# Kernel optimization log

Measured on AMD Instinct MI355X. Metric: run time of the kernel, lower is better.

Reference implementation:

```python
import jax, jax.numpy as jnp
import numpy as np

N_NODES, N_EDGES = 20000, 2000
IN_FEATS, NUM_HEADS, OUT_FEATS, EDGE_DIM = 128, 4, 32, 64
NEG_SLOPE = 0.2


def setup_inputs() -> dict:
    key = jax.random.key(0)
    ks = jax.random.split(key, 5)
    # Unique (node, edge) incidence pairs, concrete at setup time.
    rng = np.random.default_rng(0)
    flat = np.unique(rng.integers(0, N_NODES * N_EDGES, size=220000))
    src_idx = jnp.asarray(flat // N_EDGES, dtype=jnp.int32)
    edge_idx = jnp.asarray(flat % N_EDGES, dtype=jnp.int32)
    H = jnp.zeros((N_NODES, N_EDGES), jnp.float32).at[src_idx, edge_idx].set(1.0)
    feat = jax.random.normal(ks[0], (N_NODES, IN_FEATS), jnp.float32)
    edge_feat = jax.random.normal(ks[1], (N_EDGES, EDGE_DIM), jnp.float32)
    fc_w = jax.random.normal(ks[2], (IN_FEATS, NUM_HEADS * OUT_FEATS), jnp.float32) * 0.1
    attn_src = jax.random.normal(ks[3], (1, NUM_HEADS, OUT_FEATS), jnp.float32) * 0.1
    attn_edge = jax.random.normal(ks[4], (1, NUM_HEADS, EDGE_DIM), jnp.float32) * 0.1
    return {"feat": feat, "edge_feat": edge_feat, "H": H, "fc_w": fc_w,
            "attn_src": attn_src, "attn_edge": attn_edge,
            "src_idx": src_idx, "edge_idx": edge_idx}


def reference(feat, edge_feat, H, fc_w, attn_src, attn_edge, src_idx, edge_idx):
    n_nodes = feat.shape[0]
    n_edges = H.shape[1]
    # node projection -> [N, h, d]
    feat_src = (feat @ fc_w).reshape(n_nodes, NUM_HEADS, OUT_FEATS)
    # gather per incidence pair
    src_feat = feat_src[src_idx]                       # [P, h, d]
    e_src = (src_feat * attn_src).sum(-1)              # [P, h]
    e_edge = (edge_feat[edge_idx][:, None, :] * attn_edge).sum(-1)  # [P, h]
    e = jax.nn.leaky_relu(e_src + e_edge, NEG_SLOPE)   # [P, h]
    # grouped (per-hyperedge) softmax via segment ops
    max_val = jax.ops.segment_max(e, edge_idx, num_segments=n_edges)  # [E, h]
    e_exp = jnp.exp(e - max_val[edge_idx])
    sum_exp = jax.ops.segment_sum(e_exp, edge_idx, num_segments=n_edges)
    attention = e_exp / (sum_exp[edge_idx] + 1e-9)     # [P, h]
    # aggregate messages onto hyperedges
    messages = src_feat * attention[..., None]         # [P, h, d]
    hyper_edge_feats = jax.ops.segment_sum(messages, edge_idx, num_segments=n_edges)  # [E, h, d]
    # dense disseminate back to nodes
    rst = jnp.einsum('ne,ehd->nhd', H, hyper_edge_feats)
    return rst.reshape(n_nodes, NUM_HEADS * OUT_FEATS)
```

## Files before the change

### kernel.cpp

```cpp
#include <hip/hip_runtime.h>
#include <hip/hip_bf16.h>

#define N_NODES 20000
#define N_EDGES 2000
#define IN_FEATS 128
#define NUM_HEADS 4
#define OUT_FEATS 32
#define EDGE_DIM 64
#define C_FEATS 128
#define NEG_SLOPE 0.2f
#define MAXD 256
#define WT_LD 136
#define NTILES (N_NODES / 16)
#define PROJ_BLKS ((NTILES + 3) / 4)
#define K1_BLK 512
#define K1_THR 256
#define CUR_STRIDE 16

typedef __attribute__((ext_vector_type(8))) short bf16x8;
typedef __attribute__((ext_vector_type(4))) float f32x4;

__device__ __forceinline__ float leaky(float x) { return (x > 0.f) ? x : NEG_SLOPE * x; }
__device__ __forceinline__ short f2bf(float x) {
    __hip_bfloat16 h = __float2bfloat16(x);
    return *reinterpret_cast<short*>(&h);
}

__global__ __launch_bounds__(K1_THR) void proj_scatter_kernel(
    const float* __restrict__ feat, const float* __restrict__ fc_w,
    const float* __restrict__ attn_src,
    const int* __restrict__ src_idx, const int* __restrict__ edge_idx, int P,
    __hip_bfloat16* __restrict__ feat_bf, float* __restrict__ s_buf,
    int* __restrict__ cursor, int* __restrict__ node_start, int* __restrict__ edge_nodes)
{
    __shared__ unsigned short Wt[128 * WT_LD];
    const int t = threadIdx.x;
    const int bid = blockIdx.x;

    if (bid < PROJ_BLKS) {
        for (int q = t; q < 64 * 128; q += K1_THR) {
            const int c = q & 127, k = (q >> 7) * 2;
            Wt[c * WT_LD + k]     = (unsigned short)f2bf(fc_w[k * C_FEATS + c]);
            Wt[c * WT_LD + k + 1] = (unsigned short)f2bf(fc_w[(k + 1) * C_FEATS + c]);
        }
        __syncthreads();

        const int wave = t >> 6, lane = t & 63;
        const int wid = bid * 4 + wave;
        if (wid < NTILES) {
            const int m0 = wid * 16;
            const int lrow = lane & 15, lk = lane >> 4;

            bf16x8 afr[4];
            const float* arow = feat + (size_t)(m0 + lrow) * IN_FEATS + lk * 8;
            #pragma unroll
            for (int kt = 0; kt < 4; ++kt) {
                const float4 f0 = *(const float4*)(arow + kt * 32);
                const float4 f1 = *(const float4*)(arow + kt * 32 + 4);
                bf16x8 a;
                a[0] = f2bf(f0.x); a[1] = f2bf(f0.y); a[2] = f2bf(f0.z); a[3] = f2bf(f0.w);
                a[4] = f2bf(f1.x); a[5] = f2bf(f1.y); a[6] = f2bf(f1.z); a[7] = f2bf(f1.w);
                afr[kt] = a;
            }

            f32x4 acc[8];
            #pragma unroll
            for (int nt = 0; nt < 8; ++nt) acc[nt] = (f32x4){0.f, 0.f, 0.f, 0.f};
            #pragma unroll
            for (int nt = 0; nt < 8; ++nt) {
                const unsigned short* wrow = &Wt[(nt * 16 + lrow) * WT_LD + lk * 8];
                #pragma unroll
                for (int kt = 0; kt < 4; ++kt) {
                    const bf16x8 b = *(const bf16x8*)(wrow + kt * 32);
                    acc[nt] = __builtin_amdgcn_mfma_f32_16x16x32_bf16(afr[kt], b, acc[nt], 0, 0, 0);
                }
            }

            #pragma unroll
            for (int nt = 0; nt < 8; ++nt) {
                const int c = nt * 16 + lrow;
                #pragma unroll
                for (int r = 0; r < 4; ++r)
                    feat_bf[(size_t)(m0 + lk * 4 + r) * C_FEATS + c] = __float2bfloat16(acc[nt][r]);
            }
            float aw[8];
            #pragma unroll
            for (int nt = 0; nt < 8; ++nt) aw[nt] = attn_src[nt * 16 + lrow];
            #pragma unroll
            for (int h = 0; h < NUM_HEADS; ++h) {
                #pragma unroll
                for (int r = 0; r < 4; ++r) {
                    float v = acc[2 * h][r] * aw[2 * h] + acc[2 * h + 1][r] * aw[2 * h + 1];
                    v += __shfl_xor(v, 1);
                    v += __shfl_xor(v, 2);
                    v += __shfl_xor(v, 4);
                    v += __shfl_xor(v, 8);
                    if (lrow == 0) s_buf[(m0 + lk * 4 + r) * NUM_HEADS + h] = v;
                }
            }
        }
    } else {
        const int nthreads = (K1_BLK - PROJ_BLKS) * K1_THR;
        for (int p = (bid - PROJ_BLKS) * K1_THR + t; p < P; p += nthreads) {
            const int e = edge_idx[p];
            const int s = src_idx[p];
            const int pos = atomicAdd(&cursor[e * CUR_STRIDE], 1);
            if (pos < MAXD) edge_nodes[e * MAXD + pos] = s;
            const int prev = (p == 0) ? -1 : src_idx[p - 1];
            for (int n = prev + 1; n <= s; ++n) node_start[n] = p;
            if (p == P - 1)
                for (int n = s + 1; n <= N_NODES; ++n) node_start[n] = P;
        }
    }
}

__global__ __launch_bounds__(256) void edge_attn_kernel(
    const float* __restrict__ s_buf, const float* __restrict__ edge_feat,
    const float* __restrict__ attn_edge, const __hip_bfloat16* __restrict__ feat_bf,
    const int* __restrict__ cursor, const int* __restrict__ edge_nodes,
    float* __restrict__ hef)
{
    __shared__ float4 w_sh[MAXD];
    __shared__ int    n_sh[MAXD];
    __shared__ float  te_sh[NUM_HEADS];
    __shared__ float  inv_sh[NUM_HEADS];
    __shared__ float  wred[4][NUM_HEADS];
    __shared__ float  red[4][C_FEATS];

    const int e = blockIdx.x;
    const int t = threadIdx.x;
    const int wv = t >> 6, lane = t & 63;

    if (t < EDGE_DIM) {
        const float v = edge_feat[e * EDGE_DIM + t];
        #pragma unroll
        for (int h = 0; h < NUM_HEADS; ++h) {
            float p = v * attn_edge[h * EDGE_DIM + t];
            p += __shfl_xor(p, 32); p += __shfl_xor(p, 16); p += __shfl_xor(p, 8);
            p += __shfl_xor(p, 4);  p += __shfl_xor(p, 2);  p += __shfl_xor(p, 1);
            if (t == 0) te_sh[h] = p;
        }
    }
    __syncthreads();

    const int m = min(cursor[e * CUR_STRIDE], MAXD);
    const int m_pad = (m + 31) & ~31;

    float ps0 = 0.f, ps1 = 0.f, ps2 = 0.f, ps3 = 0.f;
    if (t < m) {
        const int n = edge_nodes[e * MAXD + t];
        n_sh[t] = n;
        const float4 s4 = *(const float4*)&s_buf[n * NUM_HEADS];
        float4 w;
        w.x = __expf(leaky(s4.x + te_sh[0]));
        w.y = __expf(leaky(s4.y + te_sh[1]));
        w.z = __expf(leaky(s4.z + te_sh[2]));
        w.w = __expf(leaky(s4.w + te_sh[3]));
        w_sh[t] = w;
        ps0 = w.x; ps1 = w.y; ps2 = w.z; ps3 = w.w;
    } else if (t < m_pad) {
        n_sh[t] = 0;
        w_sh[t] = make_float4(0.f, 0.f, 0.f, 0.f);
    }
    #pragma unroll
    for (int d = 32; d >= 1; d >>= 1) {
        ps0 += __shfl_xor(ps0, d); ps1 += __shfl_xor(ps1, d);
        ps2 += __shfl_xor(ps2, d); ps3 += __shfl_xor(ps3, d);
    }
    if (lane == 0) {
        wred[wv][0] = ps0; wred[wv][1] = ps1; wred[wv][2] = ps2; wred[wv][3] = ps3;
    }
    __syncthreads();
    if (t < NUM_HEADS)
        inv_sh[t] = 1.f / (wred[0][t] + wred[1][t] + wred[2][t] + wred[3][t] + 1e-9f);
    __syncthreads();

    const int c0 = lane * 2;
    const int h = lane >> 4;
    float a0 = 0.f, a1 = 0.f;
    const unsigned short* fb = (const unsigned short*)feat_bf;
    #pragma unroll 8
    for (int j = wv; j < m_pad; j += 4) {
        const int n = n_sh[j];
        const float w = ((const float*)&w_sh[j])[h];
        const unsigned v = *(const unsigned*)(fb + (size_t)n * C_FEATS + c0);
        a0 += w * __uint_as_float(v << 16);
        a1 += w * __uint_as_float(v & 0xffff0000u);
    }
    red[wv][c0] = a0;
    red[wv][c0 + 1] = a1;
    __syncthreads();
    if (t < C_FEATS) {
        const float r = red[0][t] + red[1][t] + red[2][t] + red[3][t];
        hef[e * C_FEATS + t] = r * inv_sh[t >> 5];
    }
}

#define K3_NODES 8
#define K3_CHUNK 512
__global__ __launch_bounds__(128) void disseminate_kernel(
    const int* __restrict__ node_start, const int* __restrict__ edge_idx,
    const float* __restrict__ hef, float* __restrict__ out)
{
    __shared__ int e_sh[K3_CHUNK];
    __shared__ int ns_sh[K3_NODES + 1];
    const int n0 = blockIdx.x * K3_NODES;
    const int c = threadIdx.x;
    if (c < K3_NODES + 1) ns_sh[c] = node_start[n0 + c];
    __syncthreads();
    const int s0 = ns_sh[0], s1 = ns_sh[K3_NODES];

    float acc[K3_NODES];
    #pragma unroll
    for (int r = 0; r < K3_NODES; ++r) acc[r] = 0.f;

    for (int cb = s0; cb < s1; cb += K3_CHUNK) {
        const int ccnt = min(K3_CHUNK, s1 - cb);
        __syncthreads();
        for (int i = c; i < ccnt; i += 128) e_sh[i] = edge_idx[cb + i];
        __syncthreads();
        #pragma unroll 1
        for (int r = 0; r < K3_NODES; ++r) {
            const int jlo = max(ns_sh[r], cb);
            const int jhi = min(ns_sh[r + 1], cb + ccnt);
            float a = acc[r];
            #pragma unroll 8
            for (int j = jlo; j < jhi; ++j)
                a += hef[(size_t)e_sh[j - cb] * C_FEATS + c];
            acc[r] = a;
        }
    }
    #pragma unroll
    for (int r = 0; r < K3_NODES; ++r)
        out[(size_t)(n0 + r) * C_FEATS + c] = acc[r];
}

extern "C" void kernel_launch(void* const* d_in, const int* in_sizes, int n_in,
                              void* d_out, int out_size, void* d_ws, size_t ws_size,
                              hipStream_t stream) {
    const float* feat      = (const float*)d_in[0];
    const float* edge_feat = (const float*)d_in[1];
    const float* fc_w      = (const float*)d_in[3];
    const float* attn_src  = (const float*)d_in[4];
    const float* attn_edge = (const float*)d_in[5];
    const int*   src_idx   = (const int*)d_in[6];
    const int*   edge_idx  = (const int*)d_in[7];
    const int P = in_sizes[6];
    float* out = (float*)d_out;

    float* ws = (float*)d_ws;
    float*          s_buf      = ws;
    float*          hef        = s_buf + N_NODES * NUM_HEADS;
    __hip_bfloat16* feat_bf    = (__hip_bfloat16*)(hef + N_EDGES * C_FEATS);
    int*            node_start = (int*)(feat_bf + (size_t)N_NODES * C_FEATS);
    int*            edge_nodes = node_start + (N_NODES + 1);
    int*            cursor     = edge_nodes + N_EDGES * MAXD;

    hipMemsetAsync(cursor, 0, N_EDGES * CUR_STRIDE * sizeof(int), stream);
    proj_scatter_kernel<<<K1_BLK, K1_THR, 0, stream>>>(
        feat, fc_w, attn_src, src_idx, edge_idx, P,
        feat_bf, s_buf, cursor, node_start, edge_nodes);
    edge_attn_kernel<<<N_EDGES, 256, 0, stream>>>(
        s_buf, edge_feat, attn_edge, feat_bf, cursor, edge_nodes, hef);
    disseminate_kernel<<<N_NODES / K3_NODES, 128, 0, stream>>>(
        node_start, edge_idx, hef, out);
}
```

Before: 57.11 us.

## Store hyperedge features in bf16 and widen edge-attention and disseminate blocks

```diff
diff --git a/kernel.cpp b/kernel.cpp
--- a/kernel.cpp
+++ b/kernel.cpp
@@ -114,18 +114,18 @@
     }
 }
 
-__global__ __launch_bounds__(256) void edge_attn_kernel(
+__global__ __launch_bounds__(512) void edge_attn_kernel(
     const float* __restrict__ s_buf, const float* __restrict__ edge_feat,
     const float* __restrict__ attn_edge, const __hip_bfloat16* __restrict__ feat_bf,
     const int* __restrict__ cursor, const int* __restrict__ edge_nodes,
-    float* __restrict__ hef)
+    __hip_bfloat16* __restrict__ hef)
 {
     __shared__ float4 w_sh[MAXD];
     __shared__ int    n_sh[MAXD];
     __shared__ float  te_sh[NUM_HEADS];
     __shared__ float  inv_sh[NUM_HEADS];
-    __shared__ float  wred[4][NUM_HEADS];
-    __shared__ float  red[4][C_FEATS];
+    __shared__ float  wred[8][NUM_HEADS];
+    __shared__ float  red[8][C_FEATS];
 
     const int e = blockIdx.x;
     const int t = threadIdx.x;
@@ -171,8 +171,12 @@
         wred[wv][0] = ps0; wred[wv][1] = ps1; wred[wv][2] = ps2; wred[wv][3] = ps3;
     }
     __syncthreads();
-    if (t < NUM_HEADS)
-        inv_sh[t] = 1.f / (wred[0][t] + wred[1][t] + wred[2][t] + wred[3][t] + 1e-9f);
+    if (t < NUM_HEADS) {
+        float s = 0.f;
+        #pragma unroll
+        for (int w8 = 0; w8 < 8; ++w8) s += wred[w8][t];
+        inv_sh[t] = 1.f / (s + 1e-9f);
+    }
     __syncthreads();
 
     const int c0 = lane * 2;
@@ -180,7 +184,7 @@
     float a0 = 0.f, a1 = 0.f;
     const unsigned short* fb = (const unsigned short*)feat_bf;
     #pragma unroll 8
-    for (int j = wv; j < m_pad; j += 4) {
+    for (int j = wv; j < m_pad; j += 8) {
         const int n = n_sh[j];
         const float w = ((const float*)&w_sh[j])[h];
         const unsigned v = *(const unsigned*)(fb + (size_t)n * C_FEATS + c0);
@@ -191,48 +195,63 @@
     red[wv][c0 + 1] = a1;
     __syncthreads();
     if (t < C_FEATS) {
-        const float r = red[0][t] + red[1][t] + red[2][t] + red[3][t];
-        hef[e * C_FEATS + t] = r * inv_sh[t >> 5];
+        float r = 0.f;
+        #pragma unroll
+        for (int w8 = 0; w8 < 8; ++w8) r += red[w8][t];
+        hef[e * C_FEATS + t] = __float2bfloat16(r * inv_sh[t >> 5]);
     }
 }
 
 #define K3_NODES 8
 #define K3_CHUNK 512
-__global__ __launch_bounds__(128) void disseminate_kernel(
+__global__ __launch_bounds__(256) void disseminate_kernel(
     const int* __restrict__ node_start, const int* __restrict__ edge_idx,
-    const float* __restrict__ hef, float* __restrict__ out)
+    const __hip_bfloat16* __restrict__ hef, float* __restrict__ out)
 {
     __shared__ int e_sh[K3_CHUNK];
     __shared__ int ns_sh[K3_NODES + 1];
+    const int t = threadIdx.x;
+    const int wv = t >> 6, lane = t & 63;
+    const int c0 = lane * 2;
     const int n0 = blockIdx.x * K3_NODES;
-    const int c = threadIdx.x;
-    if (c < K3_NODES + 1) ns_sh[c] = node_start[n0 + c];
+
+    if (t < K3_NODES + 1) ns_sh[t] = node_start[n0 + t];
     __syncthreads();
     const int s0 = ns_sh[0], s1 = ns_sh[K3_NODES];
 
-    float acc[K3_NODES];
-    #pragma unroll
-    for (int r = 0; r < K3_NODES; ++r) acc[r] = 0.f;
+    float a00 = 0.f, a01 = 0.f, a10 = 0.f, a11 = 0.f;
+    const unsigned short* hu = (const unsigned short*)hef;
 
     for (int cb = s0; cb < s1; cb += K3_CHUNK) {
         const int ccnt = min(K3_CHUNK, s1 - cb);
         __syncthreads();
-        for (int i = c; i < ccnt; i += 128) e_sh[i] = edge_idx[cb + i];
+        for (int i = t; i < ccnt; i += 256) e_sh[i] = edge_idx[cb + i];
         __syncthreads();
-        #pragma unroll 1
-        for (int r = 0; r < K3_NODES; ++r) {
-            const int jlo = max(ns_sh[r], cb);
-            const int jhi = min(ns_sh[r + 1], cb + ccnt);
-            float a = acc[r];
+        {
+            const int jlo = max(ns_sh[wv * 2], cb);
+            const int jhi = min(ns_sh[wv * 2 + 1], cb + ccnt);
             #pragma unroll 8
-            for (int j = jlo; j < jhi; ++j)
-                a += hef[(size_t)e_sh[j - cb] * C_FEATS + c];
-            acc[r] = a;
-        }
-    }
-    #pragma unroll
-    for (int r = 0; r < K3_NODES; ++r)
-        out[(size_t)(n0 + r) * C_FEATS + c] = acc[r];
+            for (int j = jlo; j < jhi; ++j) {
+                const unsigned v = *(const unsigned*)(hu + (size_t)e_sh[j - cb] * C_FEATS + c0);
+                a00 += __uint_as_float(v << 16);
+                a01 += __uint_as_float(v & 0xffff0000u);
+            }
+        }
+        {
+            const int jlo = max(ns_sh[wv * 2 + 1], cb);
+            const int jhi = min(ns_sh[wv * 2 + 2], cb + ccnt);
+            #pragma unroll 8
+            for (int j = jlo; j < jhi; ++j) {
+                const unsigned v = *(const unsigned*)(hu + (size_t)e_sh[j - cb] * C_FEATS + c0);
+                a10 += __uint_as_float(v << 16);
+                a11 += __uint_as_float(v & 0xffff0000u);
+            }
+        }
+    }
+    float2 r0 = make_float2(a00, a01);
+    float2 r1 = make_float2(a10, a11);
+    *(float2*)&out[(size_t)(n0 + wv * 2)     * C_FEATS + c0] = r0;
+    *(float2*)&out[(size_t)(n0 + wv * 2 + 1) * C_FEATS + c0] = r1;
 }
 
 extern "C" void kernel_launch(void* const* d_in, const int* in_sizes, int n_in,
@@ -250,8 +269,8 @@
 
     float* ws = (float*)d_ws;
     float*          s_buf      = ws;
-    float*          hef        = s_buf + N_NODES * NUM_HEADS;
-    __hip_bfloat16* feat_bf    = (__hip_bfloat16*)(hef + N_EDGES * C_FEATS);
+    __hip_bfloat16* hef        = (__hip_bfloat16*)(s_buf + N_NODES * NUM_HEADS);
+    __hip_bfloat16* feat_bf    = hef + N_EDGES * C_FEATS;
     int*            node_start = (int*)(feat_bf + (size_t)N_NODES * C_FEATS);
     int*            edge_nodes = node_start + (N_NODES + 1);
     int*            cursor     = edge_nodes + N_EDGES * MAXD;
@@ -260,8 +279,8 @@
     proj_scatter_kernel<<<K1_BLK, K1_THR, 0, stream>>>(
         feat, fc_w, attn_src, src_idx, edge_idx, P,
         feat_bf, s_buf, cursor, node_start, edge_nodes);
-    edge_attn_kernel<<<N_EDGES, 256, 0, stream>>>(
+    edge_attn_kernel<<<N_EDGES, 512, 0, stream>>>(
         s_buf, edge_feat, attn_edge, feat_bf, cursor, edge_nodes, hef);
-    disseminate_kernel<<<N_NODES / K3_NODES, 128, 0, stream>>>(
+    disseminate_kernel<<<N_NODES / K3_NODES, 256, 0, stream>>>(
         node_start, edge_idx, hef, out);
 }
```

Measured after the change: 56.42 us. Within noise of the previous version (-1.2%).
